# Optimization experiments

Hardware: AMD Instinct MI355X
Metric: run time of the kernel (lower is better)

## Reference

```python
import jax, jax.numpy as jnp
import numpy as np

B, C, H1, W1 = 64, 3, 512, 512
H2, W2 = 224, 224


def setup_inputs() -> dict:
    key = jax.random.key(0)
    # images in [0,1] as produced by ToTensor / expected by ToPILImage
    x = jax.random.uniform(key, (B, C, H1, W1), dtype=jnp.float32)
    return {"input": x}


def reference(input) -> jnp.ndarray:
    # PIL Resize (default BILINEAR) performs an antialiased bilinear resize
    # when downsampling. jax.image.resize with method='bilinear' and
    # antialias=True matches this math, applied batched over [B, C].
    out_shape = (input.shape[0], input.shape[1], H2, W2)
    return jax.image.resize(input, out_shape, method="bilinear", antialias=True)
```

## Files before the change

kernel.cpp:

```cpp
#include <hip/hip_runtime.h>

#define IN_H 512
#define IN_W 512
#define OUT_H 224
#define OUT_W 224
#define OY 8
#define NROWS 21
#define BLOCK 256


__global__ __launch_bounds__(BLOCK) void resize_aa_fused(
    const float* __restrict__ in, float* __restrict__ out) {

    __shared__ float s_in[NROWS][IN_W];
    __shared__ float s_h[NROWS][OUT_W];
    __shared__ float s_wx[OUT_W][5];
    __shared__ int   s_ix0[OUT_W];
    __shared__ float s_wy[OY][5];
    __shared__ int   s_ro[OY];

    const int bc  = blockIdx.x;
    const int oy0 = blockIdx.y * OY;
    const int tid = threadIdx.x;

    const float inv_scale = 16.f / 7.f;
    const float scl       = 7.f / 16.f;

    const int iy_first = (int)ceilf((oy0 + 0.5f) * inv_scale - 0.5f - inv_scale);

    if (tid < OUT_W) {
        float cx  = (tid + 0.5f) * inv_scale - 0.5f;
        int   ix0 = (int)ceilf(cx - inv_scale);
        float w[5];
        float s = 0.f;
#pragma unroll
        for (int j = 0; j < 5; ++j) {
            int i = ix0 + j;
            float ww = 1.f - fabsf(cx - (float)i) * scl;
            ww = fmaxf(ww, 0.f);
            if (i < 0 || i >= IN_W) ww = 0.f;
            w[j] = ww;
            s += ww;
        }
        float invs = 1.f / s;
#pragma unroll
        for (int j = 0; j < 5; ++j) s_wx[tid][j] = w[j] * invs;
        s_ix0[tid] = ix0;
    }

    if (tid < OY) {
        int   oy  = oy0 + tid;
        float cy  = (oy + 0.5f) * inv_scale - 0.5f;
        int   iy0 = (int)ceilf(cy - inv_scale);
        float w[5];
        float s = 0.f;
#pragma unroll
        for (int j = 0; j < 5; ++j) {
            int i = iy0 + j;
            float ww = 1.f - fabsf(cy - (float)i) * scl;
            ww = fmaxf(ww, 0.f);
            if (i < 0 || i >= IN_H) ww = 0.f;
            w[j] = ww;
            s += ww;
        }
        float invs = 1.f / s;
#pragma unroll
        for (int j = 0; j < 5; ++j) s_wy[tid][j] = w[j] * invs;
        s_ro[tid] = iy0 - iy_first;
    }

    const float* src = in + (size_t)bc * (IN_H * IN_W);
    for (int idx = tid; idx < NROWS * (IN_W / 4); idx += BLOCK) {
        int r  = idx >> 7;
        int c4 = idx & 127;
        int row = min(max(iy_first + r, 0), IN_H - 1);
        float4 v = ((const float4*)(src + (size_t)row * IN_W))[c4];
        ((float4*)(&s_in[r][0]))[c4] = v;
    }

    __syncthreads();

    for (int idx = tid; idx < NROWS * OUT_W; idx += BLOCK) {
        int r  = idx / OUT_W;
        int ox = idx - r * OUT_W;
        int ix0 = s_ix0[ox];
        float acc = 0.f;
#pragma unroll
        for (int j = 0; j < 5; ++j) {
            int i = min(max(ix0 + j, 0), IN_W - 1);
            acc = fmaf(s_wx[ox][j], s_in[r][i], acc);
        }
        s_h[r][ox] = acc;
    }

    __syncthreads();

    for (int idx = tid; idx < OY * OUT_W; idx += BLOCK) {
        int t  = idx / OUT_W;
        int ox = idx - t * OUT_W;
        int ro = s_ro[t];
        float acc = 0.f;
#pragma unroll
        for (int j = 0; j < 5; ++j) {
            acc = fmaf(s_wy[t][j], s_h[ro + j][ox], acc);
        }
        out[((size_t)bc * OUT_H + (oy0 + t)) * OUT_W + ox] = acc;
    }
}

extern "C" void kernel_launch(void* const* d_in, const int* in_sizes, int n_in,
                              void* d_out, int out_size, void* d_ws, size_t ws_size,
                              hipStream_t stream) {
    const float* in = (const float*)d_in[0];
    float* out = (float*)d_out;
    dim3 block(BLOCK);
    dim3 grid(64 * 3, OUT_H / OY);
    hipLaunchKernelGGL(resize_aa_fused, grid, block, 0, stream, in, out);
}
```

Measured before the change: 342.0 us.

## Apply vertical filter first straight from global memory, then horizontal in LDS

Reorders the separable filter so each thread reads 5 input rows directly from global memory as float4 and applies the vertical weights in registers. Only the 4 vertically filtered rows per block are staged in LDS before the horizontal pass. The block tile shrinks from 8 to 4 output rows, which cuts LDS use and raises occupancy. In exchange, rows shared between neighbouring output rows are re-read from global memory and rely on cache, with no LDS staging of the raw input.

```diff
diff --git a/kernel.cpp b/kernel.cpp
--- a/kernel.cpp
+++ b/kernel.cpp
@@ -4,20 +4,16 @@
 #define IN_W 512
 #define OUT_H 224
 #define OUT_W 224
-#define OY 8
-#define NROWS 21
+#define OY 4
 #define BLOCK 256
 
 
-__global__ __launch_bounds__(BLOCK) void resize_aa_fused(
+__global__ __launch_bounds__(BLOCK) void resize_aa_vfirst(
     const float* __restrict__ in, float* __restrict__ out) {
 
-    __shared__ float s_in[NROWS][IN_W];
-    __shared__ float s_h[NROWS][OUT_W];
+    __shared__ float s_v[OY][IN_W];
     __shared__ float s_wx[OUT_W][5];
     __shared__ int   s_ix0[OUT_W];
-    __shared__ float s_wy[OY][5];
-    __shared__ int   s_ro[OY];
 
     const int bc  = blockIdx.x;
     const int oy0 = blockIdx.y * OY;
@@ -25,8 +21,6 @@
 
     const float inv_scale = 16.f / 7.f;
     const float scl       = 7.f / 16.f;
-
-    const int iy_first = (int)ceilf((oy0 + 0.5f) * inv_scale - 0.5f - inv_scale);
 
     if (tid < OUT_W) {
         float cx  = (tid + 0.5f) * inv_scale - 0.5f;
@@ -48,11 +42,13 @@
         s_ix0[tid] = ix0;
     }
 
-    if (tid < OY) {
-        int   oy  = oy0 + tid;
-        float cy  = (oy + 0.5f) * inv_scale - 0.5f;
+    const float* src = in + (size_t)bc * (IN_H * IN_W);
+    for (int q = tid; q < OY * (IN_W / 4); q += BLOCK) {
+        int t  = q >> 7;
+        int x0 = (q & 127) << 2;
+        float cy  = (oy0 + t + 0.5f) * inv_scale - 0.5f;
         int   iy0 = (int)ceilf(cy - inv_scale);
-        float w[5];
+        float4 acc = make_float4(0.f, 0.f, 0.f, 0.f);
         float s = 0.f;
 #pragma unroll
         for (int j = 0; j < 5; ++j) {
@@ -60,37 +56,17 @@
             float ww = 1.f - fabsf(cy - (float)i) * scl;
             ww = fmaxf(ww, 0.f);
             if (i < 0 || i >= IN_H) ww = 0.f;
-            w[j] = ww;
             s += ww;
+            int r = min(max(i, 0), IN_H - 1);
+            float4 v = *(const float4*)(src + (size_t)r * IN_W + x0);
+            acc.x = fmaf(ww, v.x, acc.x);
+            acc.y = fmaf(ww, v.y, acc.y);
+            acc.z = fmaf(ww, v.z, acc.z);
+            acc.w = fmaf(ww, v.w, acc.w);
         }
         float invs = 1.f / s;
-#pragma unroll
-        for (int j = 0; j < 5; ++j) s_wy[tid][j] = w[j] * invs;
-        s_ro[tid] = iy0 - iy_first;
-    }
-
-    const float* src = in + (size_t)bc * (IN_H * IN_W);
-    for (int idx = tid; idx < NROWS * (IN_W / 4); idx += BLOCK) {
-        int r  = idx >> 7;
-        int c4 = idx & 127;
-        int row = min(max(iy_first + r, 0), IN_H - 1);
-        float4 v = ((const float4*)(src + (size_t)row * IN_W))[c4];
-        ((float4*)(&s_in[r][0]))[c4] = v;
-    }
-
-    __syncthreads();
-
-    for (int idx = tid; idx < NROWS * OUT_W; idx += BLOCK) {
-        int r  = idx / OUT_W;
-        int ox = idx - r * OUT_W;
-        int ix0 = s_ix0[ox];
-        float acc = 0.f;
-#pragma unroll
-        for (int j = 0; j < 5; ++j) {
-            int i = min(max(ix0 + j, 0), IN_W - 1);
-            acc = fmaf(s_wx[ox][j], s_in[r][i], acc);
-        }
-        s_h[r][ox] = acc;
+        acc.x *= invs; acc.y *= invs; acc.z *= invs; acc.w *= invs;
+        *(float4*)(&s_v[t][x0]) = acc;
     }
 
     __syncthreads();
@@ -98,11 +74,12 @@
     for (int idx = tid; idx < OY * OUT_W; idx += BLOCK) {
         int t  = idx / OUT_W;
         int ox = idx - t * OUT_W;
-        int ro = s_ro[t];
+        int ix0 = s_ix0[ox];
         float acc = 0.f;
 #pragma unroll
         for (int j = 0; j < 5; ++j) {
-            acc = fmaf(s_wy[t][j], s_h[ro + j][ox], acc);
+            int c = min(max(ix0 + j, 0), IN_W - 1);
+            acc = fmaf(s_wx[ox][j], s_v[t][c], acc);
         }
         out[((size_t)bc * OUT_H + (oy0 + t)) * OUT_W + ox] = acc;
     }
@@ -115,5 +92,5 @@
     float* out = (float*)d_out;
     dim3 block(BLOCK);
     dim3 grid(64 * 3, OUT_H / OY);
-    hipLaunchKernelGGL(resize_aa_fused, grid, block, 0, stream, in, out);
+    hipLaunchKernelGGL(resize_aa_vfirst, grid, block, 0, stream, in, out);
 }
```

Result: faster. 282.8 us (-17.3%).
